# Performance work log

Measured on AMD Instinct MI355X. Metric: run time of the kernel, lower is better.

The kernel has to match this reference:

```python
import jax, jax.numpy as jnp
import numpy as np
from jax import lax

ALPHA = 2.0   # snntorch surrogate.atan(alpha=2.0)
THR = 1.0     # snntorch Leaky default threshold
NUM_STEPS = 8

@jax.custom_vjp
def spike(x):
    # Heaviside forward, ATan surrogate backward (matches snntorch surrogate.atan)
    return (x > 0).astype(x.dtype)

def _spk_fwd(x):
    return (x > 0).astype(x.dtype), x

def _spk_bwd(x, g):
    return (g * (ALPHA / 2.0) / (1.0 + (jnp.pi / 2.0 * ALPHA * x) ** 2),)

spike.defvjp(_spk_fwd, _spk_bwd)


def setup_inputs() -> dict:
    key = jax.random.key(0)
    ks = jax.random.split(key, 7)
    B, D, H, A = 16384, 512, 2048, 8
    H2 = H // 2
    s1 = 1.0 / np.sqrt(D)
    s2 = 1.0 / np.sqrt(H)
    s3 = 1.0 / np.sqrt(H2)
    return {
        "x": jax.random.normal(ks[0], (B, D), jnp.float32),
        "W1": jax.random.uniform(ks[1], (H, D), jnp.float32, -s1, s1),
        "b1": jax.random.uniform(ks[2], (H,), jnp.float32, -s1, s1),
        "W2": jax.random.uniform(ks[3], (H2, H), jnp.float32, -s2, s2),
        "b2": jax.random.uniform(ks[4], (H2,), jnp.float32, -s2, s2),
        "Wo": jax.random.uniform(ks[5], (A, H2), jnp.float32, -s3, s3),
        "bo": jax.random.uniform(ks[6], (A,), jnp.float32, -s3, s3),
        "beta1": jnp.float32(0.9),
        "beta2": jnp.float32(0.85),
        "beta_out": jnp.float32(0.95),
    }


def reference(x, W1, b1, W2, b2, Wo, bo, beta1, beta2, beta_out):
    B = x.shape[0]
    H, H2, A = W1.shape[0], W2.shape[0], Wo.shape[0]
    # snntorch clamps learnable beta into [0, 1] inside the state function
    be1 = jnp.clip(beta1, 0.0, 1.0)
    be2 = jnp.clip(beta2, 0.0, 1.0)
    beo = jnp.clip(beta_out, 0.0, 1.0)

    cur1 = x @ W1.T + b1  # fc1(x) is identical every step; hoist out of the loop

    mem1 = jnp.zeros((B, H), x.dtype)
    mem2 = jnp.zeros((B, H2), x.dtype)
    mem_out = jnp.zeros((B, A), x.dtype)
    max_mem = jnp.full((B, A), -1e9, x.dtype)

    def step(carry, _):
        mem1, mem2, mem_out, max_mem = carry
        # lif1: subtract-reset Leaky; reset uses detached spike of previous mem
        reset1 = lax.stop_gradient(spike(mem1 - THR))
        mem1 = be1 * mem1 + cur1 - reset1 * THR
        spk1 = spike(mem1 - THR)
        # lif2
        reset2 = lax.stop_gradient(spike(mem2 - THR))
        mem2 = be2 * mem2 + (spk1 @ W2.T + b2) - reset2 * THR
        spk2 = spike(mem2 - THR)
        # li_out: reset_mechanism='none' -> pure leaky integrator
        mem_out = beo * mem_out + (spk2 @ Wo.T + bo)
        max_mem = jnp.maximum(max_mem, mem_out)
        return (mem1, mem2, mem_out, max_mem), None

    (mem1, mem2, mem_out, max_mem), _ = lax.scan(
        step, (mem1, mem2, mem_out, max_mem), None, length=NUM_STEPS
    )
    return max_mem
```

## Files before the change

### kernel.cpp

```cpp
#include <hip/hip_runtime.h>
#include <stdint.h>


typedef __bf16 bf16;
typedef __attribute__((ext_vector_type(8))) __bf16 bf16x8;
typedef __attribute__((ext_vector_type(4))) float f32x4;

#define CAP1 2097152
#define CAP2 2097152
#define MARGIN 2e-3f
#define MARGIN2 5e-4f

__device__ __forceinline__ void gl16(const void* g, void* l) {
  __builtin_amdgcn_global_load_lds(
      (const __attribute__((address_space(1))) uint32_t*)g,
      (__attribute__((address_space(3))) uint32_t*)l, 16, 0, 0);
}

__device__ __forceinline__ float clampf(float v) {
  return fminf(fmaxf(v, 0.f), 1.f);
}

__device__ __forceinline__ uint32_t expand2(uint32_t b) {
  return ((b & 1u) ? 0x3F80u : 0u) | ((b & 2u) ? 0x3F800000u : 0u);
}


__global__ void split_x_kernel(const float* __restrict__ x, bf16* __restrict__ Ax) {
  int i = blockIdx.x * 256 + threadIdx.x;
  int b = i >> 9, d = i & 511;
  float v = x[i];
  bf16 hi = (bf16)v;
  bf16 lo = (bf16)(v - (float)hi);
  size_t base = (size_t)b * 1024;
  Ax[base + d] = hi;
  Ax[base + 512 + d] = lo;
}

__global__ void split_w1_kernel(const float* __restrict__ W1, bf16* __restrict__ B0,
                                bf16* __restrict__ B1) {
  int i = blockIdx.x * 256 + threadIdx.x;
  int r = i >> 9, d = i & 511;
  float v = W1[i];
  bf16 hi = (bf16)v;
  bf16 lo = (bf16)(v - (float)hi);
  size_t base = (size_t)r * 1024;
  B0[base + d] = hi;  B0[base + 512 + d] = lo;
  B1[base + d] = lo;  B1[base + 512 + d] = hi;
}

__global__ void split_w2_kernel(const float* __restrict__ W2, bf16* __restrict__ Wh,
                                bf16* __restrict__ Wl) {
  int i = blockIdx.x * 256 + threadIdx.x;
  float v = W2[i];
  bf16 hi = (bf16)v;
  Wh[i] = hi;
  Wl[i] = (bf16)(v - (float)hi);
}


#define SA_OFF  0
#define SB0_OFF 16384
#define SB1_OFF 32768

__global__ __launch_bounds__(256, 2) void gemm1_lif1_kernel(
    const bf16* __restrict__ A, const bf16* __restrict__ B0,
    const bf16* __restrict__ B1, const float* __restrict__ bias,
    const float* __restrict__ beta1p,
    uint32_t* __restrict__ spkbits1, uint2* __restrict__ flag1,
    uint32_t* __restrict__ cnt1)
{
  __shared__ __align__(16) uint8_t lds[49152];
  const int tid = threadIdx.x;
  const int lane = tid & 63;
  const int wave = tid >> 6;
  const int wm = (wave >> 1) * 64, wn = (wave & 1) * 64;
  const size_t brow = (size_t)blockIdx.x * 128;
  const size_t bcol = (size_t)blockIdx.y * 128;
  const int K = 1024;
  const float be = clampf(beta1p[0]);

  const bf16* gA  = A  + brow * K;
  const bf16* gB0 = B0 + bcol * K;
  const bf16* gB1 = B1 + bcol * K;

  f32x4 acc[4][4] = {};

  for (int kk = 0; kk < K; kk += 64) {
#pragma unroll
    for (int q = 0; q < 4; ++q) {
      const int flat = q * 256 + tid;
      const int row = flat >> 3;
      const int s   = flat & 7;
      const int c8  = (s ^ (row & 7)) * 8;
      gl16(gA  + (size_t)row * K + kk + c8, lds + SA_OFF  + flat * 16);
      gl16(gB0 + (size_t)row * K + kk + c8, lds + SB0_OFF + flat * 16);
      gl16(gB1 + (size_t)row * K + kk + c8, lds + SB1_OFF + flat * 16);
    }
    asm volatile("s_waitcnt vmcnt(0)" ::: "memory");
    __syncthreads();
#pragma unroll
    for (int ks = 0; ks < 2; ++ks) {
      bf16x8 af[4], b0f[4], b1f[4];
#pragma unroll
      for (int i = 0; i < 4; ++i) {
        const int ra = wm + i * 16 + (lane & 15);
        const int sa = ((ks * 4 + (lane >> 4)) ^ (ra & 7)) * 16;
        af[i]  = *(const bf16x8*)(lds + SA_OFF  + ra * 128 + sa);
        const int rb = wn + i * 16 + (lane & 15);
        const int sb = ((ks * 4 + (lane >> 4)) ^ (rb & 7)) * 16;
        b0f[i] = *(const bf16x8*)(lds + SB0_OFF + rb * 128 + sb);
        b1f[i] = *(const bf16x8*)(lds + SB1_OFF + rb * 128 + sb);
      }
#pragma unroll
      for (int m = 0; m < 4; ++m)
#pragma unroll
        for (int n = 0; n < 4; ++n) {
          acc[m][n] = __builtin_amdgcn_mfma_f32_16x16x32_bf16(af[m], b0f[n], acc[m][n], 0, 0, 0);
          acc[m][n] = __builtin_amdgcn_mfma_f32_16x16x32_bf16(af[m], b1f[n], acc[m][n], 0, 0, 0);
        }
    }
    __syncthreads();
  }

  uint32_t* lcnt  = (uint32_t*)lds;
  uint32_t* lbase = (uint32_t*)(lds + 4);
  uint2*    llist = (uint2*)(lds + 16);
  const uint32_t CAPL = 3000;
  if (tid == 0) *lcnt = 0;
  __syncthreads();

  const int rg = lane >> 4;
  const bool writer = (lane & 15) == 0;
  uint16_t* sp16 = (uint16_t*)spkbits1;

#pragma unroll
  for (int m = 0; m < 4; ++m)
#pragma unroll
    for (int n = 0; n < 4; ++n) {
      const int chb = (int)(bcol) + wn + n * 16;
      const int w32 = chb >> 5, half = (chb >> 4) & 1;
      const float bv = bias[chb + (lane & 15)];
#pragma unroll
      for (int j = 0; j < 4; ++j) {
        const float c = acc[m][n][j] + bv;
        float mem = 0.f; uint32_t hist = 0; bool nearThr = false;
#pragma unroll
        for (int t = 0; t < 8; ++t) {
          float rst = (mem > 1.f) ? 1.f : 0.f;
          mem = be * mem + c - rst;
          uint32_t bit = (mem > 1.f) ? 1u : 0u;
          hist |= bit << t;
          nearThr |= (fabsf(mem - 1.f) < MARGIN);
        }
#pragma unroll
        for (int t = 0; t < 8; ++t) {
          unsigned long long bal = __ballot((hist >> t) & 1u);
          if (writer) {
            uint32_t row = (uint32_t)(brow + wm + m * 16 + rg * 4 + j);
            size_t idx = ((size_t)(t * 64 + w32) * 16384 + row) * 2 + half;
            sp16[idx] = (uint16_t)(bal >> (rg * 16));
          }
        }
        if (nearThr) {
          const uint32_t h = (uint32_t)(chb + (lane & 15));
          const uint32_t b = (uint32_t)(brow + wm + m * 16 + rg * 4 + j);
          uint2 en; en.x = (h << 14) | b; en.y = hist;
          uint32_t pos = atomicAdd(lcnt, 1u);
          if (pos < CAPL) llist[pos] = en;
          else { uint32_t g = atomicAdd(cnt1, 1u); if (g < CAP1) flag1[g] = en; }
        }
      }
    }

  __syncthreads();
  uint32_t ln = *lcnt; if (ln > CAPL) ln = CAPL;
  if (tid == 0) *lbase = atomicAdd(cnt1, ln);
  __syncthreads();
  const uint32_t gb = *lbase;
  for (uint32_t i = tid; i < ln; i += 256) {
    uint32_t g = gb + i;
    if (g < CAP1) flag1[g] = llist[i];
  }
}


__global__ __launch_bounds__(256) void repair1_kernel(
    const float* __restrict__ x, const float* __restrict__ W1,
    const float* __restrict__ b1, const float* __restrict__ beta1p,
    const uint2* __restrict__ flag1, const uint32_t* __restrict__ cnt1,
    uint32_t* __restrict__ spkbits1)
{
  uint32_t n = cnt1[0]; if (n > CAP1) n = CAP1;
  const float be = clampf(beta1p[0]);
  for (uint32_t i = blockIdx.x * 256 + threadIdx.x; i < n; i += gridDim.x * 256) {
    uint2 e = flag1[i];
    int h = e.x >> 14, b = e.x & 16383;
    const float* xr = x + (size_t)b * 512;
    const float* wr = W1 + (size_t)h * 512;
    float s = 0.f;
    for (int d = 0; d < 512; ++d) s = fmaf(xr[d], wr[d], s);
    s = __fadd_rn(s, b1[h]);
    float m = 0.f; uint32_t eb = 0;
#pragma unroll
    for (int t = 0; t < 8; ++t) {
      float rst = (__fsub_rn(m, 1.f) > 0.f) ? 1.f : 0.f;
      m = __fsub_rn(__fadd_rn(__fmul_rn(be, m), s), rst);
      if (__fsub_rn(m, 1.f) > 0.f) eb |= 1u << t;
    }
    uint32_t diff = eb ^ (e.y & 0xFFu);
    if (diff) {
#pragma unroll
      for (int t = 0; t < 8; ++t)
        if ((diff >> t) & 1u)
          atomicXor(&spkbits1[((size_t)t * 64 + (h >> 5)) * 16384 + b], 1u << (h & 31));
    }
  }
}


#define BOFF(d) ((d) * 32768)

__global__ __launch_bounds__(256, 2) void step2_kernel(
    const uint32_t* __restrict__ spkbits1,
    const bf16* __restrict__ W2h, const bf16* __restrict__ W2l,
    const float* __restrict__ b2, const float* __restrict__ beta2p,
    uint32_t* __restrict__ spkbits2, uint32_t* __restrict__ flag2,
    uint32_t* __restrict__ cnt2)
{
  __shared__ __align__(16) uint8_t lds[65536];
  const int K = 2048;
  const int tid = threadIdx.x;
  const int lane = tid & 63;
  const int wave = tid >> 6;
  const int wm = (wave >> 1) * 64, wn = (wave & 1) * 64;
  const size_t brow = (size_t)blockIdx.x * 128;
  const size_t bcol = (size_t)blockIdx.y * 128;
  const float be2 = clampf(beta2p[0]);

  const bf16* gB0 = W2h + bcol * K;
  const bf16* gB1 = W2l + bcol * K;

  float b2c[4];
#pragma unroll
  for (int n = 0; n < 4; ++n) b2c[n] = b2[bcol + wn + n * 16 + (lane & 15)];

  const int rg = lane >> 4;
  const int lnlo = lane & 15;
  const int sh8 = rg * 8;
  const bool writer = lnlo == 0;
  uint16_t* sp16 = (uint16_t*)spkbits2;

  f32x4 acc[4][4] = {};
  unsigned long long flg = 0;

#define STAGE_B(D, KKN)                                                       \
  {                                                                           \
    _Pragma("unroll")                                                         \
    for (int q = 0; q < 4; ++q) {                                             \
      const int flat = q * 256 + tid;                                         \
      const int row = flat >> 3;                                              \
      const int s = flat & 7;                                                 \
      const int c8 = (s ^ (row & 7)) * 8;                                     \
      gl16(gB0 + (size_t)row * K + (KKN) * 64 + c8, lds + BOFF(D) + flat * 16);\
      gl16(gB1 + (size_t)row * K + (KKN) * 64 + c8,                           \
           lds + BOFF(D) + 16384 + flat * 16);                                \
    }                                                                         \
  }

#define CHUNK(KK, NK, D)                                                      \
  {                                                                           \
    uint32_t aw[2][4];                                                        \
    const uint32_t* pA =                                                      \
        spkbits1 + ((size_t)(t * 64 + (KK) * 2)) * 16384 + brow;              \
    _Pragma("unroll")                                                         \
    for (int ks = 0; ks < 2; ++ks)                                            \
      _Pragma("unroll")                                                       \
      for (int i = 0; i < 4; ++i)                                             \
        aw[ks][i] = pA[(size_t)ks * 16384 + wm + i * 16 + lnlo];              \
    STAGE_B(D ^ 1, NK);                                                       \
    bf16x8 af[2][4];                                                          \
    _Pragma("unroll")                                                         \
    for (int ks = 0; ks < 2; ++ks)                                            \
      _Pragma("unroll")                                                       \
      for (int i = 0; i < 4; ++i) {                                           \
        uint32_t byte = (aw[ks][i] >> sh8) & 0xFFu;                           \
        uint4 u;                                                              \
        u.x = expand2(byte);                                                  \
        u.y = expand2(byte >> 2);                                             \
        u.z = expand2(byte >> 4);                                             \
        u.w = expand2(byte >> 6);                                             \
        af[ks][i] = *(bf16x8*)&u;                                             \
      }                                                                       \
    asm volatile("s_waitcnt vmcnt(8)" ::: "memory");                          \
    __builtin_amdgcn_s_barrier();                                             \
    _Pragma("unroll")                                                         \
    for (int ks = 0; ks < 2; ++ks) {                                          \
      bf16x8 b0f[4], b1f[4];                                                  \
      _Pragma("unroll")                                                       \
      for (int i = 0; i < 4; ++i) {                                           \
        const int rb = wn + i * 16 + lnlo;                                    \
        const int sb = ((ks * 4 + rg) ^ (rb & 7)) * 16;                       \
        b0f[i] = *(const bf16x8*)(lds + BOFF(D) + rb * 128 + sb);             \
        b1f[i] = *(const bf16x8*)(lds + BOFF(D) + 16384 + rb * 128 + sb);     \
      }                                                                       \
      _Pragma("unroll")                                                       \
      for (int m = 0; m < 4; ++m)                                             \
        _Pragma("unroll")                                                     \
        for (int n = 0; n < 4; ++n) {                                         \
          acc[m][n] = __builtin_amdgcn_mfma_f32_16x16x32_bf16(                \
              af[ks][m], b0f[n], acc[m][n], 0, 0, 0);                         \
          acc[m][n] = __builtin_amdgcn_mfma_f32_16x16x32_bf16(                \
              af[ks][m], b1f[n], acc[m][n], 0, 0, 0);                         \
        }                                                                     \
    }                                                                         \
    __builtin_amdgcn_s_barrier();                                             \
  }

  STAGE_B(0, 0);

  for (int t = 0; t < 8; ++t) {
#pragma unroll
    for (int m = 0; m < 4; ++m)
#pragma unroll
      for (int n = 0; n < 4; ++n)
#pragma unroll
        for (int j = 0; j < 4; ++j) {
          float v = acc[m][n][j];
          float rst = (v > 1.f) ? 1.f : 0.f;
          acc[m][n][j] = be2 * v + (b2c[n] - rst);
        }

#pragma unroll 1
    for (int kk2 = 0; kk2 < 16; ++kk2) {
      CHUNK(2 * kk2,     (2 * kk2 + 1) & 31, 0)
      CHUNK(2 * kk2 + 1, (2 * kk2 + 2) & 31, 1)
    }

#pragma unroll
    for (int m = 0; m < 4; ++m)
#pragma unroll
      for (int n = 0; n < 4; ++n) {
        const int chb = (int)(bcol) + wn + n * 16;
        const int w32 = chb >> 5, half = (chb >> 4) & 1;
#pragma unroll
        for (int j = 0; j < 4; ++j) {
          float v = acc[m][n][j];
          if (fabsf(v - 1.f) < MARGIN2) flg |= 1ull << (m * 16 + n * 4 + j);
          unsigned long long bal = __ballot(v > 1.f);
          if (writer) {
            uint32_t row = (uint32_t)(brow + wm + m * 16 + rg * 4 + j);
            size_t idx = ((size_t)(t * 32 + w32) * 16384 + row) * 2 + half;
            sp16[idx] = (uint16_t)(bal >> (rg * 16));
          }
        }
      }
  }

  __syncthreads();
  uint32_t* lcnt  = (uint32_t*)lds;
  uint32_t* lbase = (uint32_t*)(lds + 4);
  uint32_t* llist = (uint32_t*)(lds + 16);
  const uint32_t CAPL = 6000;
  if (tid == 0) *lcnt = 0;
  __syncthreads();

  if (flg) {
#pragma unroll
    for (int m = 0; m < 4; ++m)
#pragma unroll
      for (int n = 0; n < 4; ++n)
#pragma unroll
        for (int j = 0; j < 4; ++j)
          if ((flg >> (m * 16 + n * 4 + j)) & 1ull) {
            const int row = wm + m * 16 + rg * 4 + j;
            const int col = wn + n * 16 + lnlo;
            uint32_t en = (uint32_t)(((brow + row) << 10) | (bcol + col));
            uint32_t pos = atomicAdd(lcnt, 1u);
            if (pos < CAPL) llist[pos] = en;
            else { uint32_t g = atomicAdd(cnt2, 1u); if (g < CAP2) flag2[g] = en; }
          }
  }

  __syncthreads();
  uint32_t ln = *lcnt; if (ln > CAPL) ln = CAPL;
  if (tid == 0) *lbase = atomicAdd(cnt2, ln);
  __syncthreads();
  const uint32_t gb = *lbase;
  for (uint32_t i = tid; i < ln; i += 256) {
    uint32_t g = gb + i;
    if (g < CAP2) flag2[g] = llist[i];
  }
#undef STAGE_B
#undef CHUNK
}


__global__ __launch_bounds__(256) void repair2_kernel(
    const uint32_t* __restrict__ spkbits1, const float* __restrict__ W2,
    const float* __restrict__ b2, const float* __restrict__ beta2p,
    const uint32_t* __restrict__ flag2, const uint32_t* __restrict__ cnt2,
    uint32_t* __restrict__ spkbits2)
{
  uint32_t n = cnt2[0]; if (n > CAP2) n = CAP2;
  const float be = clampf(beta2p[0]);
  for (uint32_t i = blockIdx.x * 256 + threadIdx.x; i < n; i += gridDim.x * 256) {
    uint32_t e = flag2[i];
    int b = e >> 10, h2 = e & 1023;
    const float* wr = W2 + (size_t)h2 * 2048;
    const float bias = b2[h2];
    float s[8] = {0, 0, 0, 0, 0, 0, 0, 0};
    for (int w = 0; w < 64; ++w) {
      uint32_t bt[8];
#pragma unroll
      for (int t = 0; t < 8; ++t)
        bt[t] = spkbits1[((size_t)t * 64 + w) * 16384 + b];
#pragma unroll 8
      for (int k = 0; k < 32; ++k) {
        const float wv = wr[w * 32 + k];
#pragma unroll
        for (int t = 0; t < 8; ++t) {
          float addend = ((bt[t] >> k) & 1u) ? wv : 0.0f;
          s[t] = __fadd_rn(s[t], addend);
        }
      }
    }
    float m = 0.f;
#pragma unroll
    for (int t = 0; t < 8; ++t) {
      float st = __fadd_rn(s[t], bias);
      float rst = (__fsub_rn(m, 1.f) > 0.f) ? 1.f : 0.f;
      m = __fsub_rn(__fadd_rn(__fmul_rn(be, m), st), rst);
      uint32_t exact = (__fsub_rn(m, 1.f) > 0.f) ? 1u : 0u;
      uint32_t* wp = &spkbits2[((size_t)t * 32 + (h2 >> 5)) * 16384 + b];
      uint32_t stored = (*wp >> (h2 & 31)) & 1u;
      if (stored != exact) atomicXor(wp, 1u << (h2 & 31));
    }
  }
}


__global__ __launch_bounds__(256) void out_kernel(
    const uint32_t* __restrict__ spkbits2, const float* __restrict__ Wo,
    const float* __restrict__ bo, const float* __restrict__ betaop,
    float* __restrict__ out)
{
  const int wave = threadIdx.x >> 6, lane = threadIdx.x & 63;
  const int b = blockIdx.x * 4 + wave;
  const float beo = clampf(betaop[0]);
  const int a = lane & 7;
  const int slice = lane >> 3;

  float s[8] = {0, 0, 0, 0, 0, 0, 0, 0};
#pragma unroll
  for (int q = 0; q < 4; ++q) {
    const int wrd = slice * 4 + q;
    uint32_t wt[8];
#pragma unroll
    for (int t = 0; t < 8; ++t)
      wt[t] = spkbits2[((size_t)(t * 32 + wrd)) * 16384 + b];
    const float* wop = Wo + (size_t)a * 1024 + wrd * 32;
#pragma unroll
    for (int k8 = 0; k8 < 8; ++k8) {
      const float4 wv = *(const float4*)(wop + k8 * 4);
      const float wa[4] = {wv.x, wv.y, wv.z, wv.w};
#pragma unroll
      for (int kk = 0; kk < 4; ++kk) {
        const int k = k8 * 4 + kk;
#pragma unroll
        for (int t = 0; t < 8; ++t)
          s[t] += ((wt[t] >> k) & 1u) ? wa[kk] : 0.0f;
      }
    }
  }
#pragma unroll
  for (int t = 0; t < 8; ++t) {
    s[t] += __shfl_down(s[t], 8, 64);
    s[t] += __shfl_down(s[t], 16, 64);
    s[t] += __shfl_down(s[t], 32, 64);
  }
  if (lane < 8) {
    const float bov = bo[a];
    float mo = 0.f, mx = -1e30f;
#pragma unroll
    for (int t = 0; t < 8; ++t) {
      mo = beo * mo + (s[t] + bov);
      mx = fmaxf(mx, mo);
    }
    out[(size_t)b * 8 + a] = mx;
  }
}

__global__ void zero_hdr_kernel(uint32_t* p) {
  if (threadIdx.x < 64) p[threadIdx.x] = 0;
}

__global__ void fill_sentinel(float* out, int n, float v) {
  int i = blockIdx.x * 256 + threadIdx.x;
  if (i < n) out[i] = v;
}


extern "C" void kernel_launch(void* const* d_in, const int* in_sizes, int n_in,
                              void* d_out, int out_size, void* d_ws, size_t ws_size,
                              hipStream_t stream)
{
  (void)in_sizes; (void)n_in;
  const float* x   = (const float*)d_in[0];
  const float* W1  = (const float*)d_in[1];
  const float* b1  = (const float*)d_in[2];
  const float* W2  = (const float*)d_in[3];
  const float* b2  = (const float*)d_in[4];
  const float* Wo  = (const float*)d_in[5];
  const float* bo  = (const float*)d_in[6];
  const float* be1 = (const float*)d_in[7];
  const float* be2 = (const float*)d_in[8];
  const float* beo = (const float*)d_in[9];
  float* out = (float*)d_out;

  const int B = 16384, D = 512, H = 2048, H2 = 1024;

  const size_t sz_hdr  = 256;
  const size_t sz_Ax   = (size_t)B * 1024 * 2;
  const size_t sz_W1s  = (size_t)H * 1024 * 2;
  const size_t sz_W2s  = (size_t)H2 * H * 2;
  const size_t sz_b1   = (size_t)8 * 64 * B * 4;
  const size_t sz_b2   = (size_t)8 * 32 * B * 4;
  const size_t sz_f1   = (size_t)CAP1 * 8;
  const size_t sz_f2   = (size_t)CAP2 * 4;
  const size_t need = sz_hdr + sz_Ax + 2 * sz_W1s + 2 * sz_W2s +
                      sz_b1 + sz_b2 + sz_f1 + sz_f2;

  if (ws_size < need) {
    fill_sentinel<<<(out_size + 255) / 256, 256, 0, stream>>>(
        out, out_size, 1000.0f + (float)(ws_size >> 20));
    return;
  }

  uint8_t* p = (uint8_t*)d_ws;
  uint32_t* hdr = (uint32_t*)p;     p += sz_hdr;
  bf16* Ax      = (bf16*)p;         p += sz_Ax;
  bf16* W1B0    = (bf16*)p;         p += sz_W1s;
  bf16* W1B1    = (bf16*)p;         p += sz_W1s;
  bf16* W2h     = (bf16*)p;         p += sz_W2s;
  bf16* W2l     = (bf16*)p;         p += sz_W2s;
  uint32_t* spkbits1 = (uint32_t*)p; p += sz_b1;
  uint32_t* spkbits2 = (uint32_t*)p; p += sz_b2;
  uint2* flag1  = (uint2*)p;        p += sz_f1;
  uint32_t* flag2 = (uint32_t*)p;   p += sz_f2;
  uint32_t* cnt1 = hdr + 0;
  uint32_t* cnt2 = hdr + 1;

  zero_hdr_kernel<<<1, 64, 0, stream>>>(hdr);
  split_x_kernel <<<(B * D) / 256, 256, 0, stream>>>(x, Ax);
  split_w1_kernel<<<(H * D) / 256, 256, 0, stream>>>(W1, W1B0, W1B1);
  split_w2_kernel<<<(H2 * H) / 256, 256, 0, stream>>>(W2, W2h, W2l);

  gemm1_lif1_kernel<<<dim3(B / 128, H / 128), 256, 0, stream>>>(
      Ax, W1B0, W1B1, b1, be1, spkbits1, flag1, cnt1);
  repair1_kernel<<<256, 256, 0, stream>>>(x, W1, b1, be1, flag1, cnt1, spkbits1);

  step2_kernel<<<dim3(B / 128, H2 / 128), 256, 0, stream>>>(
      spkbits1, W2h, W2l, b2, be2, spkbits2, flag2, cnt2);
  repair2_kernel<<<256, 256, 0, stream>>>(spkbits1, W2, b2, be2, flag2, cnt2, spkbits2);

  out_kernel<<<B / 4, 256, 0, stream>>>(spkbits2, Wo, bo, beo, out);
}
```

Measured before the change: 1.710 ms.

## Halve step2 K-chunk and LDS to fit four blocks per CU, prefetch spike words

The layer-2 spiking GEMM now stages 32-wide K chunks of the hi/lo bf16 W2 tiles instead of 64-wide ones. This halves shared memory to 32KB so the launch bound can ask for four blocks per CU instead of two. The spike-bit A words are loaded one chunk ahead into alternating register sets, including across timestep boundaries, so their global latency overlaps the MFMA work. In exchange, barriers per unit of work double, and the tighter register budget may cause spills given the 64-float accumulator tile. A final vmcnt(0) drain is added before the LDS is reused for the flag list.

```diff
diff --git a/kernel.cpp b/kernel.cpp
--- a/kernel.cpp
+++ b/kernel.cpp
@@ -219,16 +219,16 @@
 }
 
 
-#define BOFF(d) ((d) * 32768)
-
-__global__ __launch_bounds__(256, 2) void step2_kernel(
+#define BOFF(d) ((d) * 16384)
+
+__global__ __launch_bounds__(256, 4) void step2_kernel(
     const uint32_t* __restrict__ spkbits1,
     const bf16* __restrict__ W2h, const bf16* __restrict__ W2l,
     const float* __restrict__ b2, const float* __restrict__ beta2p,
     uint32_t* __restrict__ spkbits2, uint32_t* __restrict__ flag2,
     uint32_t* __restrict__ cnt2)
 {
-  __shared__ __align__(16) uint8_t lds[65536];
+  __shared__ __align__(16) uint8_t lds[32768];
   const int K = 2048;
   const int tid = threadIdx.x;
   const int lane = tid & 63;
@@ -254,69 +254,68 @@
   f32x4 acc[4][4] = {};
   unsigned long long flg = 0;
 
-#define STAGE_B(D, KKN)                                                       \
+#define STAGE_B(D, KC)                                                        \
   {                                                                           \
     _Pragma("unroll")                                                         \
-    for (int q = 0; q < 4; ++q) {                                             \
+    for (int q = 0; q < 2; ++q) {                                             \
       const int flat = q * 256 + tid;                                         \
-      const int row = flat >> 3;                                              \
-      const int s = flat & 7;                                                 \
-      const int c8 = (s ^ (row & 7)) * 8;                                     \
-      gl16(gB0 + (size_t)row * K + (KKN) * 64 + c8, lds + BOFF(D) + flat * 16);\
-      gl16(gB1 + (size_t)row * K + (KKN) * 64 + c8,                           \
-           lds + BOFF(D) + 16384 + flat * 16);                                \
+      const int row = flat >> 2;                                              \
+      const int s = flat & 3;                                                 \
+      const int c8 = (s ^ ((row >> 1) & 3)) * 8;                              \
+      gl16(gB0 + (size_t)row * K + (KC) * 32 + c8, lds + BOFF(D) + flat * 16);\
+      gl16(gB1 + (size_t)row * K + (KC) * 32 + c8,                            \
+           lds + BOFF(D) + 8192 + flat * 16);                                 \
     }                                                                         \
   }
 
-#define CHUNK(KK, NK, D)                                                      \
+#define LOAD_A(AW, TT, KC)                                                    \
   {                                                                           \
-    uint32_t aw[2][4];                                                        \
     const uint32_t* pA =                                                      \
-        spkbits1 + ((size_t)(t * 64 + (KK) * 2)) * 16384 + brow;              \
+        spkbits1 + ((size_t)((TT) * 64 + (KC))) * 16384 + brow;               \
     _Pragma("unroll")                                                         \
-    for (int ks = 0; ks < 2; ++ks)                                            \
-      _Pragma("unroll")                                                       \
-      for (int i = 0; i < 4; ++i)                                             \
-        aw[ks][i] = pA[(size_t)ks * 16384 + wm + i * 16 + lnlo];              \
-    STAGE_B(D ^ 1, NK);                                                       \
-    bf16x8 af[2][4];                                                          \
+    for (int i = 0; i < 4; ++i) AW[i] = pA[wm + i * 16 + lnlo];               \
+  }
+
+#define CHUNK(CUR, NXT, TT_N, KC_N, D)                                        \
+  {                                                                           \
+    LOAD_A(NXT, TT_N, KC_N);                                                  \
+    STAGE_B(D ^ 1, KC_N);                                                     \
+    bf16x8 af[4];                                                             \
     _Pragma("unroll")                                                         \
-    for (int ks = 0; ks < 2; ++ks)                                            \
-      _Pragma("unroll")                                                       \
-      for (int i = 0; i < 4; ++i) {                                           \
-        uint32_t byte = (aw[ks][i] >> sh8) & 0xFFu;                           \
-        uint4 u;                                                              \
-        u.x = expand2(byte);                                                  \
-        u.y = expand2(byte >> 2);                                             \
-        u.z = expand2(byte >> 4);                                             \
-        u.w = expand2(byte >> 6);                                             \
-        af[ks][i] = *(bf16x8*)&u;                                             \
-      }                                                                       \
+    for (int i = 0; i < 4; ++i) {                                             \
+      uint32_t byte = (CUR[i] >> sh8) & 0xFFu;                                \
+      uint4 u;                                                                \
+      u.x = expand2(byte);                                                    \
+      u.y = expand2(byte >> 2);                                               \
+      u.z = expand2(byte >> 4);                                               \
+      u.w = expand2(byte >> 6);                                               \
+      af[i] = *(bf16x8*)&u;                                                   \
+    }                                                                         \
     asm volatile("s_waitcnt vmcnt(8)" ::: "memory");                          \
     __builtin_amdgcn_s_barrier();                                             \
+    bf16x8 b0f[4], b1f[4];                                                    \
     _Pragma("unroll")                                                         \
-    for (int ks = 0; ks < 2; ++ks) {                                          \
-      bf16x8 b0f[4], b1f[4];                                                  \
+    for (int i = 0; i < 4; ++i) {                                             \
+      const int rb = wn + i * 16 + lnlo;                                      \
+      const int sb = (rg ^ ((rb >> 1) & 3)) * 16;                             \
+      b0f[i] = *(const bf16x8*)(lds + BOFF(D) + rb * 64 + sb);                \
+      b1f[i] = *(const bf16x8*)(lds + BOFF(D) + 8192 + rb * 64 + sb);         \
+    }                                                                         \
+    _Pragma("unroll")                                                         \
+    for (int m = 0; m < 4; ++m)                                               \
       _Pragma("unroll")                                                       \
-      for (int i = 0; i < 4; ++i) {                                           \
-        const int rb = wn + i * 16 + lnlo;                                    \
-        const int sb = ((ks * 4 + rg) ^ (rb & 7)) * 16;                       \
-        b0f[i] = *(const bf16x8*)(lds + BOFF(D) + rb * 128 + sb);             \
-        b1f[i] = *(const bf16x8*)(lds + BOFF(D) + 16384 + rb * 128 + sb);     \
+      for (int n = 0; n < 4; ++n) {                                           \
+        acc[m][n] = __builtin_amdgcn_mfma_f32_16x16x32_bf16(                  \
+            af[m], b0f[n], acc[m][n], 0, 0, 0);                               \
+        acc[m][n] = __builtin_amdgcn_mfma_f32_16x16x32_bf16(                  \
+            af[m], b1f[n], acc[m][n], 0, 0, 0);                               \
       }                                                                       \
-      _Pragma("unroll")                                                       \
-      for (int m = 0; m < 4; ++m)                                             \
-        _Pragma("unroll")                                                     \
-        for (int n = 0; n < 4; ++n) {                                         \
-          acc[m][n] = __builtin_amdgcn_mfma_f32_16x16x32_bf16(                \
-              af[ks][m], b0f[n], acc[m][n], 0, 0, 0);                         \
-          acc[m][n] = __builtin_amdgcn_mfma_f32_16x16x32_bf16(                \
-              af[ks][m], b1f[n], acc[m][n], 0, 0, 0);                         \
-        }                                                                     \
-    }                                                                         \
     __builtin_amdgcn_s_barrier();                                             \
   }
 
+  uint32_t awA[4], awB[4];
+
+  LOAD_A(awA, 0, 0);
   STAGE_B(0, 0);
 
   for (int t = 0; t < 8; ++t) {
@@ -332,9 +331,13 @@
         }
 
 #pragma unroll 1
-    for (int kk2 = 0; kk2 < 16; ++kk2) {
-      CHUNK(2 * kk2,     (2 * kk2 + 1) & 31, 0)
-      CHUNK(2 * kk2 + 1, (2 * kk2 + 2) & 31, 1)
+    for (int kc2 = 0; kc2 < 32; ++kc2) {
+      CHUNK(awA, awB, t, 2 * kc2 + 1, 0)
+      {
+        const int kcn = (2 * kc2 + 2) & 63;
+        const int tn = (kc2 == 31 && t < 7) ? t + 1 : t;
+        CHUNK(awB, awA, tn, kcn, 1)
+      }
     }
 
 #pragma unroll
@@ -357,6 +360,7 @@
       }
   }
 
+  asm volatile("s_waitcnt vmcnt(0)" ::: "memory");
   __syncthreads();
   uint32_t* lcnt  = (uint32_t*)lds;
   uint32_t* lbase = (uint32_t*)(lds + 4);
@@ -392,6 +396,7 @@
     if (g < CAP2) flag2[g] = llist[i];
   }
 #undef STAGE_B
+#undef LOAD_A
 #undef CHUNK
 }
 
```

Measured after the change: 2.421 ms. +41.6%, slower.
